# Kernel optimization log

Hardware: AMD Instinct MI355X
Metric: run time of the kernel (lower is better)

Reference implementation:

```python
import jax, jax.numpy as jnp
import numpy as np

DIM_EMB = 1024
DIM_K = 128
DIM_V = 128
BATCH = 4
SEQ = 4096

def setup_inputs() -> dict:
    key = jax.random.key(0)
    kx, kq, kk, kv = jax.random.split(key, 4)
    x = jax.random.normal(kx, (BATCH, SEQ, DIM_EMB), dtype=jnp.float32)
    Wq = jax.random.normal(kq, (DIM_EMB, DIM_K), dtype=jnp.float32) * (1.0 / np.sqrt(DIM_EMB))
    Wk = jax.random.normal(kk, (DIM_EMB, DIM_K), dtype=jnp.float32) * (1.0 / np.sqrt(DIM_EMB))
    Wv = jax.random.normal(kv, (DIM_EMB, DIM_V), dtype=jnp.float32) * (1.0 / np.sqrt(DIM_EMB))
    return {"x": x, "Wq": Wq, "Wk": Wk, "Wv": Wv}

def reference(x, Wq, Wk, Wv):
    # x: [b, s, e]; projections (torch Linear without bias -> x @ W)
    seq_len = x.shape[1]
    q = x @ Wq  # [b, s, dk]
    k = x @ Wk  # [b, s, dk]
    v = x @ Wv  # [b, s, dv]
    # NOTE: original scales by 1/sqrt(dim_emb), not 1/sqrt(dim_k)
    scale = 1.0 / np.sqrt(x.shape[-1])
    qk = jnp.einsum('bqd,bkd->bqk', q, k) * scale  # [b, s, s]
    causal = jnp.tril(jnp.ones((seq_len, seq_len), dtype=bool))
    masked_qk = jnp.where(causal, qk, -jnp.inf)
    att = jax.nn.softmax(masked_qk, axis=-1)  # dropout p=0.0 -> identity
    return att @ v  # [b, s, dv]
```

## Files before the change

### kernel.cpp

```cpp
#include <hip/hip_runtime.h>

typedef __attribute__((ext_vector_type(8))) short s8v;
typedef __attribute__((ext_vector_type(4))) short s4v;
typedef __attribute__((ext_vector_type(4))) float f4v;

#define S_ 4096
#define E_ 1024
#define D_ 128

__device__ __forceinline__ unsigned short f2bf(float f) {
  unsigned int u = __float_as_uint(f);
  return (unsigned short)((u + 0x7FFFu + ((u >> 16) & 1u)) >> 16);
}

__device__ __forceinline__ void gload16(const void* g, void* l) {
  __builtin_amdgcn_global_load_lds(
      (const __attribute__((address_space(1))) unsigned int*)g,
      (__attribute__((address_space(3))) unsigned int*)l, 16, 0, 0);
}

__global__ __launch_bounds__(256) void zero_kernel(float* __restrict__ p) {
  const int i = blockIdx.x * 256 + threadIdx.x;
  float4 z = {0.f, 0.f, 0.f, 0.f};
  reinterpret_cast<float4*>(p)[i] = z;
}

__global__ __launch_bounds__(256) void xcvt_kernel(
    const float* __restrict__ x, unsigned short* __restrict__ Xb) {
  const size_t i = ((size_t)blockIdx.x * 256 + threadIdx.x) * 8;
  float4 a = *reinterpret_cast<const float4*>(x + i);
  float4 b = *reinterpret_cast<const float4*>(x + i + 4);
  s8v v;
  v[0] = (short)f2bf(a.x); v[1] = (short)f2bf(a.y);
  v[2] = (short)f2bf(a.z); v[3] = (short)f2bf(a.w);
  v[4] = (short)f2bf(b.x); v[5] = (short)f2bf(b.y);
  v[6] = (short)f2bf(b.z); v[7] = (short)f2bf(b.w);
  *reinterpret_cast<s8v*>(Xb + i) = v;
}

__global__ __launch_bounds__(256) void wcvt_kernel(
    const float* __restrict__ Wq, const float* __restrict__ Wk,
    const float* __restrict__ Wv, unsigned short* __restrict__ Wt) {
  __shared__ unsigned short T[64][72];
  const int p = blockIdx.y;
  const float* W = (p == 0) ? Wq : (p == 1) ? Wk : Wv;
  const int k0 = (blockIdx.x >> 1) * 64;
  const int n0 = (blockIdx.x & 1) * 64;
  const int t = threadIdx.x, rr = t >> 4, c4 = (t & 15) * 4;
#pragma unroll
  for (int i = 0; i < 4; ++i) {
    int kr = i * 16 + rr;
    float4 w = *reinterpret_cast<const float4*>(W + (size_t)(k0 + kr) * D_ + n0 + c4);
    T[c4 + 0][kr] = f2bf(w.x); T[c4 + 1][kr] = f2bf(w.y);
    T[c4 + 2][kr] = f2bf(w.z); T[c4 + 3][kr] = f2bf(w.w);
  }
  __syncthreads();
#pragma unroll
  for (int i = 0; i < 4; ++i) {
    int n = i * 16 + rr;
    s4v v;
    v[0] = (short)T[n][c4]; v[1] = (short)T[n][c4 + 1];
    v[2] = (short)T[n][c4 + 2]; v[3] = (short)T[n][c4 + 3];
    *reinterpret_cast<s4v*>(Wt + (size_t)(p * D_ + n0 + n) * E_ + k0 + c4) = v;
  }
}

__global__ __launch_bounds__(256) void proj_kernel(
    const unsigned short* __restrict__ Xb, const unsigned short* __restrict__ Wt,
    unsigned short* __restrict__ Qb, unsigned short* __restrict__ Kb,
    unsigned short* __restrict__ VT) {
  __shared__ __align__(16) unsigned short As[128 * 64];
  __shared__ __align__(16) unsigned short Bs[128 * 64];
  const int bid = blockIdx.x;
  const int cls = bid & 7, j = bid >> 3;
  const int m0 = (cls * 16 + j / 3) * 128, ng = j % 3;
  const int t = threadIdx.x;
  const int wv = t >> 6, lane = t & 63, quad = lane >> 4, l16 = lane & 15;
  const int wr = wv >> 1, wc = wv & 1;

  f4v acc[4][4];
  const f4v fz = {0.f, 0.f, 0.f, 0.f};
#pragma unroll
  for (int i = 0; i < 4; ++i)
#pragma unroll
    for (int k = 0; k < 4; ++k) acc[i][k] = fz;

  const int rbase = wv * 32 + (lane >> 3);
  const int scb = ((lane & 7) ^ (lane >> 3)) * 16;
  const char* aSrc = (const char*)(Xb + (size_t)(m0 + rbase) * E_) + scb;
  const char* bSrc = (const char*)(Wt + (size_t)(ng * 128 + rbase) * E_) + scb;
  char* aDst = (char*)As + wv * 4096;
  char* bDst = (char*)Bs + wv * 4096;

  const int xm = (l16 & 7) * 16;
  const char* Ab = (const char*)As + (wr * 64 + l16) * 128;
  const char* Bb = (const char*)Bs + (wc * 64 + l16) * 128;

  for (int kk = 0; kk < E_; kk += 64) {
#pragma unroll
    for (int i = 0; i < 4; ++i)
      gload16(aSrc + (size_t)i * (8 * E_ * 2) + kk * 2, aDst + i * 1024);
#pragma unroll
    for (int i = 0; i < 4; ++i)
      gload16(bSrc + (size_t)i * (8 * E_ * 2) + kk * 2, bDst + i * 1024);
    __syncthreads();
#pragma unroll
    for (int ks = 0; ks < 2; ++ks) {
      const int co = (ks * 64 + quad * 16) ^ xm;
      s8v af[4], bf[4];
#pragma unroll
      for (int rt = 0; rt < 4; ++rt)
        af[rt] = *reinterpret_cast<const s8v*>(Ab + rt * 16 * 128 + co);
#pragma unroll
      for (int ct = 0; ct < 4; ++ct)
        bf[ct] = *reinterpret_cast<const s8v*>(Bb + ct * 16 * 128 + co);
#pragma unroll
      for (int rt = 0; rt < 4; ++rt)
#pragma unroll
        for (int ct = 0; ct < 4; ++ct)
          acc[rt][ct] = __builtin_amdgcn_mfma_f32_16x16x32_bf16(
              af[rt], bf[ct], acc[rt][ct], 0, 0, 0);
    }
    __syncthreads();
  }

  if (ng < 2) {
    unsigned short* dst = ng ? Kb : Qb;
#pragma unroll
    for (int rt = 0; rt < 4; ++rt)
#pragma unroll
      for (int ct = 0; ct < 4; ++ct)
#pragma unroll
        for (int r = 0; r < 4; ++r)
          dst[(size_t)(m0 + wr * 64 + rt * 16 + quad * 4 + r) * D_ +
              wc * 64 + ct * 16 + l16] = f2bf(acc[rt][ct][r]);
  } else {
    const int b = m0 >> 12;
    const int s0 = (m0 & (S_ - 1)) + wr * 64;
#pragma unroll
    for (int rt = 0; rt < 4; ++rt)
#pragma unroll
      for (int ct = 0; ct < 4; ++ct) {
        s4v v;
        v[0] = (short)f2bf(acc[rt][ct][0]); v[1] = (short)f2bf(acc[rt][ct][1]);
        v[2] = (short)f2bf(acc[rt][ct][2]); v[3] = (short)f2bf(acc[rt][ct][3]);
        *reinterpret_cast<s4v*>(
            VT + ((size_t)b * D_ + wc * 64 + ct * 16 + l16) * S_ + s0 +
            rt * 16 + quad * 4) = v;
      }
  }
}

__global__ __launch_bounds__(256, 4) void flash_kernel(
    const unsigned short* __restrict__ Qb, const unsigned short* __restrict__ Kb,
    const unsigned short* __restrict__ VT, float* __restrict__ Oacc,
    float* __restrict__ Lacc) {
  __shared__ __align__(16) unsigned short KS[64 * 128];
  __shared__ __align__(16) unsigned short VS[128 * 72];
  const int id = blockIdx.x;
  const int xcd = id & 7;
  const int b = xcd >> 1;
  const int sub = 287 - ((id >> 3) * 2 + (xcd & 1));
  int g = 0;
#pragma unroll
  for (int gg = 0; gg < 7; ++gg)
    if (sub >= 4 * (gg + 1) * (gg + 2)) g = gg + 1;
  const int off = sub - 4 * g * (g + 1);
  const int qt = 8 * g + off / (g + 1);
  const int s = off % (g + 1);
  const int q0 = qt * 64;
  const int klo = s * 512;
  const int khi = min((s + 1) * 512, (qt + 1) * 64);

  const int t = threadIdx.x;
  const int wv = t >> 6, lane = t & 63, quad = lane >> 4, l16 = lane & 15;
  const int qrow0 = q0 + wv * 16;
  const float SCL2 = 0.03125f * 1.44269504088896340736f;

  const unsigned short* Kbb = Kb + (size_t)b * S_ * D_;
  const unsigned short* Vbb = VT + (size_t)b * D_ * S_;

  s8v Qf[4];
#pragma unroll
  for (int ks = 0; ks < 4; ++ks)
    Qf[ks] = *reinterpret_cast<const s8v*>(
        Qb + ((size_t)b * S_ + qrow0 + l16) * D_ + ks * 32 + quad * 8);

  f4v O[8];
  const f4v fz = {0.f, 0.f, 0.f, 0.f};
#pragma unroll
  for (int nt = 0; nt < 8; ++nt) O[nt] = fz;
  float lt = 0.f;

  const int krow = t >> 4, kgb = t & 15;
  const int vrow = t >> 1, vgb = (t & 1) * 4;

  s8v kr[4], vr[4];
#pragma unroll
  for (int i = 0; i < 4; ++i) {
    kr[i] = *reinterpret_cast<const s8v*>(
        Kbb + (size_t)(klo + krow + 16 * i) * D_ + kgb * 8);
    vr[i] = *reinterpret_cast<const s8v*>(
        Vbb + (size_t)vrow * S_ + klo + (vgb + i) * 8);
  }

  for (int k0 = klo; k0 < khi; k0 += 64) {
    __syncthreads();
#pragma unroll
    for (int i = 0; i < 4; ++i) {
      const int r = krow + 16 * i;
      const int sig = (krow & 3) | ((((krow >> 3) + 2 * i) & 3) << 2);
      *reinterpret_cast<s8v*>(KS + r * 128 + ((kgb ^ sig) * 8)) = kr[i];
      *reinterpret_cast<s8v*>(VS + vrow * 72 + (vgb + i) * 8) = vr[i];
    }
    __syncthreads();
    if (k0 + 64 < khi) {
#pragma unroll
      for (int i = 0; i < 4; ++i) {
        kr[i] = *reinterpret_cast<const s8v*>(
            Kbb + (size_t)(k0 + 64 + krow + 16 * i) * D_ + kgb * 8);
        vr[i] = *reinterpret_cast<const s8v*>(
            Vbb + (size_t)vrow * S_ + k0 + 64 + (vgb + i) * 8);
      }
    }

    if (k0 <= qrow0 + 15) {
      f4v St[2][2];
#pragma unroll
      for (int c = 0; c < 2; ++c)
#pragma unroll
        for (int s2 = 0; s2 < 2; ++s2) St[c][s2] = fz;
#pragma unroll
      for (int ks = 0; ks < 4; ++ks)
#pragma unroll
        for (int c = 0; c < 2; ++c)
#pragma unroll
          for (int s2 = 0; s2 < 2; ++s2) {
            const int row = c * 32 + ((l16 >> 2) << 3) + s2 * 4 + (l16 & 3);
            s8v kf = *reinterpret_cast<const s8v*>(
                KS + row * 128 + (((ks * 4 + quad) ^ l16) * 8));
            St[c][s2] = __builtin_amdgcn_mfma_f32_16x16x32_bf16(
                kf, Qf[ks], St[c][s2], 0, 0, 0);
          }
      const bool full = (k0 + 63 <= qrow0);
      s8v pf[2];
#pragma unroll
      for (int c = 0; c < 2; ++c) {
        float ladd = 0.f;
#pragma unroll
        for (int s2 = 0; s2 < 2; ++s2)
#pragma unroll
          for (int r = 0; r < 4; ++r) {
            float e = exp2f(St[c][s2][r] * SCL2);
            if (!full) {
              int key = k0 + c * 32 + quad * 8 + s2 * 4 + r;
              if (key > qrow0 + l16) e = 0.f;
            }
            ladd += e;
            pf[c][s2 * 4 + r] = (short)f2bf(e);
          }
        lt += ladd;
      }
#pragma unroll
      for (int c = 0; c < 2; ++c)
#pragma unroll
        for (int nt = 0; nt < 8; ++nt) {
          s8v vf = *reinterpret_cast<const s8v*>(
              VS + (nt * 16 + l16) * 72 + (c * 4 + quad) * 8);
          O[nt] = __builtin_amdgcn_mfma_f32_16x16x32_bf16(
              pf[c], vf, O[nt], 0, 0, 0);
        }
    }
  }

  lt += __shfl_xor(lt, 16);
  lt += __shfl_xor(lt, 32);
  float* Ob = Oacc + (size_t)b * S_ * D_;
#pragma unroll
  for (int nt = 0; nt < 8; ++nt)
#pragma unroll
    for (int r = 0; r < 4; ++r)
      atomicAdd(&Ob[(size_t)(qrow0 + quad * 4 + r) * D_ + nt * 16 + l16],
                O[nt][r]);
  if (lane < 16) atomicAdd(&Lacc[(size_t)b * S_ + qrow0 + l16], lt);
}

__global__ __launch_bounds__(256) void norm_kernel(
    const float* __restrict__ Oacc, const float* __restrict__ Lacc,
    float* __restrict__ out) {
  const int idx = blockIdx.x * 256 + threadIdx.x;
  const int base = idx * 4;
  const int row = base >> 7;
  float4 o = reinterpret_cast<const float4*>(Oacc)[idx];
  float L = Lacc[row];
  float4 r;
  r.x = o.x / L; r.y = o.y / L; r.z = o.z / L; r.w = o.w / L;
  reinterpret_cast<float4*>(out)[idx] = r;
}

extern "C" void kernel_launch(void* const* d_in, const int* in_sizes, int n_in,
                              void* d_out, int out_size, void* d_ws, size_t ws_size,
                              hipStream_t stream) {
  const float* x = (const float*)d_in[0];
  const float* Wq = (const float*)d_in[1];
  const float* Wk = (const float*)d_in[2];
  const float* Wv = (const float*)d_in[3];
  float* out = (float*)d_out;

  char* ws = (char*)d_ws;
  unsigned short* Qb = (unsigned short*)ws;
  unsigned short* Kb = (unsigned short*)(ws + (((size_t)4) << 20));
  unsigned short* VT = (unsigned short*)(ws + (((size_t)8) << 20));
  unsigned short* Wt = (unsigned short*)(ws + (((size_t)12) << 20));
  unsigned short* Xb = (unsigned short*)(ws + (((size_t)13) << 20));
  float* Oacc = (float*)(ws + (((size_t)13) << 20));
  float* Lacc = (float*)(ws + (((size_t)21) << 20));

  wcvt_kernel<<<dim3(32, 3), 256, 0, stream>>>(Wq, Wk, Wv, Wt);
  xcvt_kernel<<<8192, 256, 0, stream>>>(x, Xb);
  proj_kernel<<<384, 256, 0, stream>>>(Xb, Wt, Qb, Kb, VT);
  zero_kernel<<<2064, 256, 0, stream>>>(Oacc);
  flash_kernel<<<1152, 256, 0, stream>>>(Qb, Kb, VT, Oacc, Lacc);
  norm_kernel<<<2048, 256, 0, stream>>>(Oacc, Lacc, out);
}
```

Baseline: 200.2 us.

## Replace atomic split-K accumulation with partial buffers, merge prep kernels, halve proj tiles

Several changes at once. The flash kernel now writes each split's partial O and L to its own slot instead of using atomicAdd, so the zero kernel is gone and the norm kernel sums the partials. The x and W conversion kernels are merged into one launch. The projection GEMM uses 128x64 tiles with 768 blocks for more parallelism, and s_setprio hints are placed around the MFMA sections. This trades atomic traffic and two launches for extra partial-buffer memory and reads in the norm kernel.

```diff
diff --git a/kernel.cpp b/kernel.cpp
--- a/kernel.cpp
+++ b/kernel.cpp
@@ -19,133 +19,132 @@
       (__attribute__((address_space(3))) unsigned int*)l, 16, 0, 0);
 }
 
-__global__ __launch_bounds__(256) void zero_kernel(float* __restrict__ p) {
-  const int i = blockIdx.x * 256 + threadIdx.x;
-  float4 z = {0.f, 0.f, 0.f, 0.f};
-  reinterpret_cast<float4*>(p)[i] = z;
-}
-
-__global__ __launch_bounds__(256) void xcvt_kernel(
-    const float* __restrict__ x, unsigned short* __restrict__ Xb) {
-  const size_t i = ((size_t)blockIdx.x * 256 + threadIdx.x) * 8;
-  float4 a = *reinterpret_cast<const float4*>(x + i);
-  float4 b = *reinterpret_cast<const float4*>(x + i + 4);
-  s8v v;
-  v[0] = (short)f2bf(a.x); v[1] = (short)f2bf(a.y);
-  v[2] = (short)f2bf(a.z); v[3] = (short)f2bf(a.w);
-  v[4] = (short)f2bf(b.x); v[5] = (short)f2bf(b.y);
-  v[6] = (short)f2bf(b.z); v[7] = (short)f2bf(b.w);
-  *reinterpret_cast<s8v*>(Xb + i) = v;
-}
-
-__global__ __launch_bounds__(256) void wcvt_kernel(
-    const float* __restrict__ Wq, const float* __restrict__ Wk,
-    const float* __restrict__ Wv, unsigned short* __restrict__ Wt) {
+__device__ __forceinline__ int slot_off(int s) { return s * (3840 - 256 * s); }
+
+__global__ __launch_bounds__(256) void prep_kernel(
+    const float* __restrict__ x, const float* __restrict__ Wq,
+    const float* __restrict__ Wk, const float* __restrict__ Wv,
+    unsigned short* __restrict__ Xb, unsigned short* __restrict__ Wt) {
   __shared__ unsigned short T[64][72];
-  const int p = blockIdx.y;
-  const float* W = (p == 0) ? Wq : (p == 1) ? Wk : Wv;
-  const int k0 = (blockIdx.x >> 1) * 64;
-  const int n0 = (blockIdx.x & 1) * 64;
-  const int t = threadIdx.x, rr = t >> 4, c4 = (t & 15) * 4;
-#pragma unroll
-  for (int i = 0; i < 4; ++i) {
-    int kr = i * 16 + rr;
-    float4 w = *reinterpret_cast<const float4*>(W + (size_t)(k0 + kr) * D_ + n0 + c4);
-    T[c4 + 0][kr] = f2bf(w.x); T[c4 + 1][kr] = f2bf(w.y);
-    T[c4 + 2][kr] = f2bf(w.z); T[c4 + 3][kr] = f2bf(w.w);
-  }
-  __syncthreads();
-#pragma unroll
-  for (int i = 0; i < 4; ++i) {
-    int n = i * 16 + rr;
-    s4v v;
-    v[0] = (short)T[n][c4]; v[1] = (short)T[n][c4 + 1];
-    v[2] = (short)T[n][c4 + 2]; v[3] = (short)T[n][c4 + 3];
-    *reinterpret_cast<s4v*>(Wt + (size_t)(p * D_ + n0 + n) * E_ + k0 + c4) = v;
-  }
-}
-
-__global__ __launch_bounds__(256) void proj_kernel(
+  const int bid = blockIdx.x;
+  if (bid < 8192) {
+    const size_t i = ((size_t)bid * 256 + threadIdx.x) * 8;
+    float4 a = *reinterpret_cast<const float4*>(x + i);
+    float4 c = *reinterpret_cast<const float4*>(x + i + 4);
+    s8v v;
+    v[0] = (short)f2bf(a.x); v[1] = (short)f2bf(a.y);
+    v[2] = (short)f2bf(a.z); v[3] = (short)f2bf(a.w);
+    v[4] = (short)f2bf(c.x); v[5] = (short)f2bf(c.y);
+    v[6] = (short)f2bf(c.z); v[7] = (short)f2bf(c.w);
+    *reinterpret_cast<s8v*>(Xb + i) = v;
+  } else {
+    const int w = bid - 8192;
+    const int p = w >> 5, bx = w & 31;
+    const float* W = (p == 0) ? Wq : (p == 1) ? Wk : Wv;
+    const int k0 = (bx >> 1) * 64;
+    const int n0 = (bx & 1) * 64;
+    const int t = threadIdx.x, rr = t >> 4, c4 = (t & 15) * 4;
+#pragma unroll
+    for (int i = 0; i < 4; ++i) {
+      int kr = i * 16 + rr;
+      float4 ww = *reinterpret_cast<const float4*>(W + (size_t)(k0 + kr) * D_ + n0 + c4);
+      T[c4 + 0][kr] = f2bf(ww.x); T[c4 + 1][kr] = f2bf(ww.y);
+      T[c4 + 2][kr] = f2bf(ww.z); T[c4 + 3][kr] = f2bf(ww.w);
+    }
+    __syncthreads();
+#pragma unroll
+    for (int i = 0; i < 4; ++i) {
+      int n = i * 16 + rr;
+      s4v v;
+      v[0] = (short)T[n][c4]; v[1] = (short)T[n][c4 + 1];
+      v[2] = (short)T[n][c4 + 2]; v[3] = (short)T[n][c4 + 3];
+      *reinterpret_cast<s4v*>(Wt + (size_t)(p * D_ + n0 + n) * E_ + k0 + c4) = v;
+    }
+  }
+}
+
+__global__ __launch_bounds__(256, 3) void proj_kernel(
     const unsigned short* __restrict__ Xb, const unsigned short* __restrict__ Wt,
     unsigned short* __restrict__ Qb, unsigned short* __restrict__ Kb,
     unsigned short* __restrict__ VT) {
   __shared__ __align__(16) unsigned short As[128 * 64];
-  __shared__ __align__(16) unsigned short Bs[128 * 64];
+  __shared__ __align__(16) unsigned short Bs[64 * 64];
   const int bid = blockIdx.x;
   const int cls = bid & 7, j = bid >> 3;
-  const int m0 = (cls * 16 + j / 3) * 128, ng = j % 3;
+  const int m0 = (cls * 16 + j / 6) * 128, ng = j % 6;
   const int t = threadIdx.x;
   const int wv = t >> 6, lane = t & 63, quad = lane >> 4, l16 = lane & 15;
   const int wr = wv >> 1, wc = wv & 1;
 
-  f4v acc[4][4];
+  f4v acc[4][2];
   const f4v fz = {0.f, 0.f, 0.f, 0.f};
 #pragma unroll
   for (int i = 0; i < 4; ++i)
 #pragma unroll
-    for (int k = 0; k < 4; ++k) acc[i][k] = fz;
-
-  const int rbase = wv * 32 + (lane >> 3);
-  const int scb = ((lane & 7) ^ (lane >> 3)) * 16;
-  const char* aSrc = (const char*)(Xb + (size_t)(m0 + rbase) * E_) + scb;
-  const char* bSrc = (const char*)(Wt + (size_t)(ng * 128 + rbase) * E_) + scb;
+    for (int k = 0; k < 2; ++k) acc[i][k] = fz;
+
+  const int lrow = lane >> 3;
+  const int scb = ((lane & 7) ^ lrow) * 16;
+  const char* aSrc = (const char*)(Xb + (size_t)(m0 + wv * 32 + lrow) * E_) + scb;
+  const char* bSrc = (const char*)(Wt + (size_t)(ng * 64 + wv * 16 + lrow) * E_) + scb;
   char* aDst = (char*)As + wv * 4096;
-  char* bDst = (char*)Bs + wv * 4096;
+  char* bDst = (char*)Bs + wv * 2048;
 
   const int xm = (l16 & 7) * 16;
   const char* Ab = (const char*)As + (wr * 64 + l16) * 128;
-  const char* Bb = (const char*)Bs + (wc * 64 + l16) * 128;
+  const char* Bb = (const char*)Bs + (wc * 32 + l16) * 128;
 
   for (int kk = 0; kk < E_; kk += 64) {
 #pragma unroll
     for (int i = 0; i < 4; ++i)
-      gload16(aSrc + (size_t)i * (8 * E_ * 2) + kk * 2, aDst + i * 1024);
-#pragma unroll
-    for (int i = 0; i < 4; ++i)
-      gload16(bSrc + (size_t)i * (8 * E_ * 2) + kk * 2, bDst + i * 1024);
+      gload16(aSrc + (size_t)(i * 8 * E_ + kk) * 2, aDst + i * 1024);
+#pragma unroll
+    for (int i = 0; i < 2; ++i)
+      gload16(bSrc + (size_t)(i * 8 * E_ + kk) * 2, bDst + i * 1024);
     __syncthreads();
 #pragma unroll
     for (int ks = 0; ks < 2; ++ks) {
       const int co = (ks * 64 + quad * 16) ^ xm;
-      s8v af[4], bf[4];
+      s8v af[4], bf[2];
 #pragma unroll
       for (int rt = 0; rt < 4; ++rt)
-        af[rt] = *reinterpret_cast<const s8v*>(Ab + rt * 16 * 128 + co);
-#pragma unroll
-      for (int ct = 0; ct < 4; ++ct)
-        bf[ct] = *reinterpret_cast<const s8v*>(Bb + ct * 16 * 128 + co);
+        af[rt] = *reinterpret_cast<const s8v*>(Ab + rt * 2048 + co);
+#pragma unroll
+      for (int ct = 0; ct < 2; ++ct)
+        bf[ct] = *reinterpret_cast<const s8v*>(Bb + ct * 2048 + co);
 #pragma unroll
       for (int rt = 0; rt < 4; ++rt)
 #pragma unroll
-        for (int ct = 0; ct < 4; ++ct)
+        for (int ct = 0; ct < 2; ++ct)
           acc[rt][ct] = __builtin_amdgcn_mfma_f32_16x16x32_bf16(
               af[rt], bf[ct], acc[rt][ct], 0, 0, 0);
     }
     __syncthreads();
   }
 
-  if (ng < 2) {
-    unsigned short* dst = ng ? Kb : Qb;
+  const int p = ng >> 1, n0 = (ng & 1) * 64;
+  if (p < 2) {
+    unsigned short* dst = p ? Kb : Qb;
 #pragma unroll
     for (int rt = 0; rt < 4; ++rt)
 #pragma unroll
-      for (int ct = 0; ct < 4; ++ct)
+      for (int ct = 0; ct < 2; ++ct)
 #pragma unroll
         for (int r = 0; r < 4; ++r)
           dst[(size_t)(m0 + wr * 64 + rt * 16 + quad * 4 + r) * D_ +
-              wc * 64 + ct * 16 + l16] = f2bf(acc[rt][ct][r]);
+              n0 + wc * 32 + ct * 16 + l16] = f2bf(acc[rt][ct][r]);
   } else {
     const int b = m0 >> 12;
     const int s0 = (m0 & (S_ - 1)) + wr * 64;
 #pragma unroll
     for (int rt = 0; rt < 4; ++rt)
 #pragma unroll
-      for (int ct = 0; ct < 4; ++ct) {
+      for (int ct = 0; ct < 2; ++ct) {
         s4v v;
         v[0] = (short)f2bf(acc[rt][ct][0]); v[1] = (short)f2bf(acc[rt][ct][1]);
         v[2] = (short)f2bf(acc[rt][ct][2]); v[3] = (short)f2bf(acc[rt][ct][3]);
         *reinterpret_cast<s4v*>(
-            VT + ((size_t)b * D_ + wc * 64 + ct * 16 + l16) * S_ + s0 +
+            VT + ((size_t)b * D_ + n0 + wc * 32 + ct * 16 + l16) * S_ + s0 +
             rt * 16 + quad * 4) = v;
       }
   }
@@ -153,8 +152,8 @@
 
 __global__ __launch_bounds__(256, 4) void flash_kernel(
     const unsigned short* __restrict__ Qb, const unsigned short* __restrict__ Kb,
-    const unsigned short* __restrict__ VT, float* __restrict__ Oacc,
-    float* __restrict__ Lacc) {
+    const unsigned short* __restrict__ VT, float* __restrict__ Op,
+    float* __restrict__ Lp) {
   __shared__ __align__(16) unsigned short KS[64 * 128];
   __shared__ __align__(16) unsigned short VS[128 * 72];
   const int id = blockIdx.x;
@@ -230,6 +229,7 @@
       for (int c = 0; c < 2; ++c)
 #pragma unroll
         for (int s2 = 0; s2 < 2; ++s2) St[c][s2] = fz;
+      __builtin_amdgcn_s_setprio(1);
 #pragma unroll
       for (int ks = 0; ks < 4; ++ks)
 #pragma unroll
@@ -242,6 +242,7 @@
             St[c][s2] = __builtin_amdgcn_mfma_f32_16x16x32_bf16(
                 kf, Qf[ks], St[c][s2], 0, 0, 0);
           }
+      __builtin_amdgcn_s_setprio(0);
       const bool full = (k0 + 63 <= qrow0);
       s8v pf[2];
 #pragma unroll
@@ -261,6 +262,7 @@
           }
         lt += ladd;
       }
+      __builtin_amdgcn_s_setprio(1);
 #pragma unroll
       for (int c = 0; c < 2; ++c)
 #pragma unroll
@@ -270,31 +272,39 @@
           O[nt] = __builtin_amdgcn_mfma_f32_16x16x32_bf16(
               pf[c], vf, O[nt], 0, 0, 0);
         }
+      __builtin_amdgcn_s_setprio(0);
     }
   }
 
   lt += __shfl_xor(lt, 16);
   lt += __shfl_xor(lt, 32);
-  float* Ob = Oacc + (size_t)b * S_ * D_;
+  const int soff = slot_off(s);
 #pragma unroll
   for (int nt = 0; nt < 8; ++nt)
 #pragma unroll
     for (int r = 0; r < 4; ++r)
-      atomicAdd(&Ob[(size_t)(qrow0 + quad * 4 + r) * D_ + nt * 16 + l16],
-                O[nt][r]);
-  if (lane < 16) atomicAdd(&Lacc[(size_t)b * S_ + qrow0 + l16], lt);
+      Op[((size_t)(qrow0 + quad * 4 + r + soff) * 4 + b) * D_ + nt * 16 + l16] =
+          O[nt][r];
+  if (lane < 16) Lp[(size_t)(qrow0 + l16 + soff) * 4 + b] = lt;
 }
 
 __global__ __launch_bounds__(256) void norm_kernel(
-    const float* __restrict__ Oacc, const float* __restrict__ Lacc,
+    const float* __restrict__ Op, const float* __restrict__ Lp,
     float* __restrict__ out) {
   const int idx = blockIdx.x * 256 + threadIdx.x;
-  const int base = idx * 4;
-  const int row = base >> 7;
-  float4 o = reinterpret_cast<const float4*>(Oacc)[idx];
-  float L = Lacc[row];
+  const int rowg = idx >> 5, d4 = idx & 31;
+  const int b = rowg >> 12, row = rowg & 4095;
+  const int g = row >> 9;
+  float ax = 0.f, ay = 0.f, az = 0.f, aw = 0.f, L = 0.f;
+  for (int s = 0; s <= g; ++s) {
+    const size_t pr = (size_t)(row + slot_off(s)) * 4 + b;
+    float4 o = reinterpret_cast<const float4*>(Op + pr * D_)[d4];
+    ax += o.x; ay += o.y; az += o.z; aw += o.w;
+    L += Lp[pr];
+  }
   float4 r;
-  r.x = o.x / L; r.y = o.y / L; r.z = o.z / L; r.w = o.w / L;
+  const float inv = 1.f / L;
+  r.x = ax * inv; r.y = ay * inv; r.z = az * inv; r.w = aw * inv;
   reinterpret_cast<float4*>(out)[idx] = r;
 }
 
@@ -313,13 +323,11 @@
   unsigned short* VT = (unsigned short*)(ws + (((size_t)8) << 20));
   unsigned short* Wt = (unsigned short*)(ws + (((size_t)12) << 20));
   unsigned short* Xb = (unsigned short*)(ws + (((size_t)13) << 20));
-  float* Oacc = (float*)(ws + (((size_t)13) << 20));
-  float* Lacc = (float*)(ws + (((size_t)21) << 20));
-
-  wcvt_kernel<<<dim3(32, 3), 256, 0, stream>>>(Wq, Wk, Wv, Wt);
-  xcvt_kernel<<<8192, 256, 0, stream>>>(x, Xb);
-  proj_kernel<<<384, 256, 0, stream>>>(Xb, Wt, Qb, Kb, VT);
-  zero_kernel<<<2064, 256, 0, stream>>>(Oacc);
-  flash_kernel<<<1152, 256, 0, stream>>>(Qb, Kb, VT, Oacc, Lacc);
-  norm_kernel<<<2048, 256, 0, stream>>>(Oacc, Lacc, out);
-}
+  float* Op = (float*)(ws + (((size_t)13) << 20));
+  float* Lp = (float*)(ws + (((size_t)50) << 20));
+
+  prep_kernel<<<8288, 256, 0, stream>>>(x, Wq, Wk, Wv, Xb, Wt);
+  proj_kernel<<<768, 256, 0, stream>>>(Xb, Wt, Qb, Kb, VT);
+  flash_kernel<<<1152, 256, 0, stream>>>(Qb, Kb, VT, Op, Lp);
+  norm_kernel<<<2048, 256, 0, stream>>>(Op, Lp, out);
+}
```

Result: faster. 167.8 us (-16.2%).
